# Optimization experiments

Hardware: AMD Instinct MI355X
Metric: run time of the kernel (lower is better)

Reference implementation:

```python
import jax, jax.numpy as jnp
import numpy as np

TEMPERATURE = 0.1
NUM_GROUPS = 1024  # must match fill_max of `groups`


def setup_inputs() -> dict:
    key = jax.random.key(0)
    k1, k2, k3 = jax.random.split(key, 3)
    B, N, D = 16, 16384, 128
    embeddings = jax.random.normal(k1, (B, N, D), dtype=jnp.float32)
    groups = jax.random.randint(k2, (B, N), 0, NUM_GROUPS, dtype=jnp.int32)
    mask = jax.random.randint(k3, (B, N), 0, 2, dtype=jnp.int32).astype(bool)
    return {"embeddings": embeddings, "groups": groups, "mask": mask}


def reference(embeddings, groups, mask):
    # Vectorized equivalent of the per-group python loop:
    # sort nodes by group, positives = roll-by-1 within each group block,
    # negatives = uniform sample from the complement of the anchor's group.
    B, N, D = embeddings.shape
    G = NUM_GROUPS
    emb = embeddings.reshape(B * N, D)
    g = groups.reshape(B * N)
    m = mask.reshape(B * N)
    total = B * N

    # masked-out nodes get sentinel group G -> sorted to the tail, excluded everywhere
    g_eff = jnp.where(m, g, G).astype(jnp.int32)
    order = jnp.argsort(g_eff)            # stable sort by group
    sg = g_eff[order]                     # sorted group labels
    counts = jax.ops.segment_sum(jnp.ones(total, jnp.int32), g_eff,
                                 num_segments=G + 1)
    starts = jnp.searchsorted(sg, jnp.arange(G + 1, dtype=jnp.int32))
    valid_total = total - counts[G]       # number of unmasked nodes

    gi = sg                               # group of element at each sorted position
    cnt = counts[gi]
    st = starts[gi]
    local = jnp.arange(total, dtype=jnp.int32) - st
    # positive partner: previous element in group, wrapping (torch.roll shifts=1)
    partner_local = jnp.mod(local - 1, jnp.maximum(cnt, 1))
    pos_idx = order[st + partner_local]
    anchor_idx = order

    # negative: uniform index into complement (all unmasked nodes not in group gi)
    comp = jnp.maximum(valid_total - cnt, 1)
    u = jax.random.uniform(jax.random.key(42), (total,))
    r = jnp.minimum((u * comp.astype(jnp.float32)).astype(jnp.int32), comp - 1)
    neg_pos = jnp.where(r < st, r, r + cnt)          # skip this group's block
    neg_idx = order[jnp.clip(neg_pos, 0, total - 1)]

    valid = (gi < G) & (cnt >= 2) & ((valid_total - cnt) > 0)

    a = emb[anchor_idx]
    p = emb[pos_idx]
    n = emb[neg_idx]
    pos_score = jnp.sum(a * p, axis=1) / TEMPERATURE
    neg_score = jnp.sum(a * n, axis=1) / TEMPERATURE
    # CE with label 0 over logits [pos, neg]: -log_softmax(...)[0]
    loss_i = jnp.logaddexp(pos_score, neg_score) - pos_score
    vw = valid.astype(loss_i.dtype)
    loss = jnp.sum(loss_i * vw) / jnp.maximum(jnp.sum(vw), 1.0)
    return loss
```

## Files before the change

kernel.cpp:

```cpp
#include <hip/hip_runtime.h>
#include <stdint.h>

#define TOTAL  262144
#define HALF   131072
#define G      1024
#define NBINS  1025
#define NCHUNK 512
#define CHUNK  512

#define OFF_COUNTS 0
#define OFF_STARTS 8192
#define OFF_FLAG   16384
#define OFF_VT     16388
#define OFF_LOSS   16392
#define OFF_VALID  16400
#define OFF_ORDER  16448
#define OFF_GHIST  1065024

__device__ __forceinline__ void threefry2x32(uint32_t k0, uint32_t k1,
                                             uint32_t& x0, uint32_t& x1) {
  uint32_t ks0 = k0, ks1 = k1, ks2 = k0 ^ k1 ^ 0x1BD11BDAu;
#define TF_RND(R) { x0 += x1; x1 = (x1 << (R)) | (x1 >> (32 - (R))); x1 ^= x0; }
  x0 += ks0; x1 += ks1;
  TF_RND(13) TF_RND(15) TF_RND(26) TF_RND(6)
  x0 += ks1; x1 += ks2 + 1u;
  TF_RND(17) TF_RND(29) TF_RND(16) TF_RND(24)
  x0 += ks2; x1 += ks0 + 2u;
  TF_RND(13) TF_RND(15) TF_RND(26) TF_RND(6)
  x0 += ks0; x1 += ks1 + 3u;
  TF_RND(17) TF_RND(29) TF_RND(16) TF_RND(24)
  x0 += ks1; x1 += ks2 + 4u;
  TF_RND(13) TF_RND(15) TF_RND(26) TF_RND(6)
  x0 += ks2; x1 += ks0 + 5u;
#undef TF_RND
}

__device__ __forceinline__ int load_mask(const void* mask, int is8, int j) {
  return is8 ? (int)((const unsigned char*)mask)[j] : ((const int*)mask)[j];
}

__global__ void k_probe_mask(const unsigned char* mb, int* flag) {
  int t = threadIdx.x;
  if ((t & 3) != 0 && mb[t] != 0) atomicOr(flag, 1);
}

__global__ __launch_bounds__(CHUNK) void k_hist(const int* __restrict__ groups,
                                                const void* __restrict__ mask,
                                                const int* __restrict__ flag,
                                                int* __restrict__ counts,
                                                int* __restrict__ ghist) {
  __shared__ int h[NBINS];
  int t = threadIdx.x;
  for (int b = t; b < NBINS; b += CHUNK) h[b] = 0;
  __syncthreads();
  int is8 = *flag;
  int j = blockIdx.x * CHUNK + t;
  int m = load_mask(mask, is8, j);
  int g = m ? groups[j] : G;
  atomicAdd(&h[g], 1);
  __syncthreads();
  for (int b = t; b < NBINS; b += CHUNK) {
    int v = h[b];
    ghist[b * NCHUNK + blockIdx.x] = v;
    if (v) atomicAdd(&counts[b], v);
  }
}

__global__ __launch_bounds__(64) void k_scan(const int* __restrict__ counts,
                                             int* __restrict__ starts,
                                             int* __restrict__ vt) {
  int l = threadIdx.x;
  int c[16];
  int s = 0;
#pragma unroll
  for (int k = 0; k < 16; k++) { c[k] = counts[l * 16 + k]; s += c[k]; }
  int incl = s;
  for (int d = 1; d < 64; d <<= 1) {
    int tt = __shfl_up(incl, d);
    if (l >= d) incl += tt;
  }
  int run = incl - s;
#pragma unroll
  for (int k = 0; k < 16; k++) { starts[l * 16 + k] = run; run += c[k]; }
  if (l == 63) starts[1024] = run;
  if (l == 0) *vt = TOTAL - counts[1024];
}

__global__ __launch_bounds__(256) void k_rebase(const int* __restrict__ starts,
                                                int* __restrict__ ghist) {
  int wave = threadIdx.x >> 6, lane = threadIdx.x & 63;
  int g = blockIdx.x * 4 + wave;
  if (g >= NBINS) return;
  int* row = ghist + g * NCHUNK;
  int v[8];
  int s = 0;
  int bi = lane * 8;
#pragma unroll
  for (int k = 0; k < 8; k++) { v[k] = row[bi + k]; s += v[k]; }
  int incl = s;
  for (int d = 1; d < 64; d <<= 1) {
    int tt = __shfl_up(incl, d);
    if (lane >= d) incl += tt;
  }
  int run = starts[g] + (incl - s);
#pragma unroll
  for (int k = 0; k < 8; k++) { int tt = v[k]; row[bi + k] = run; run += tt; }
}

__global__ __launch_bounds__(CHUNK) void k_scatter(const int* __restrict__ groups,
                                                   const void* __restrict__ mask,
                                                   const int* __restrict__ flag,
                                                   const int* __restrict__ ghist,
                                                   int* __restrict__ order) {
  __shared__ int gl[CHUNK];
  int t = threadIdx.x;
  int is8 = *flag;
  int j = blockIdx.x * CHUNK + t;
  int m = load_mask(mask, is8, j);
  int g = m ? groups[j] : G;
  gl[t] = g;
  __syncthreads();
  int rank = 0;
  for (int t2 = 0; t2 < t; t2++)
    rank += (gl[t2] == g) ? 1 : 0;
  int pos = ghist[g * NCHUNK + blockIdx.x] + rank;
  order[pos] = j;
}

__global__ __launch_bounds__(256) void k_main(const float* __restrict__ emb,
                                              const int* __restrict__ groups,
                                              const void* __restrict__ mask,
                                              const int* __restrict__ flag,
                                              const int* __restrict__ counts,
                                              const int* __restrict__ starts,
                                              const int* __restrict__ vtp,
                                              const int* __restrict__ order,
                                              double* __restrict__ lossAcc,
                                              double* __restrict__ validAcc) {
  __shared__ int mA[256], mP[256], mN[256], mV[256];
  int t = threadIdx.x;
  int i = blockIdx.x * 256 + t;
  int is8 = *flag;
  int j = order[i];
  int mm = load_mask(mask, is8, j);
  int g = mm ? groups[j] : G;
  int cnt = counts[g], st = starts[g];
  int local = i - st;
  int partner = (local == 0) ? (cnt - 1) : (local - 1);
  int pos_idx = order[st + partner];

  uint32_t x0, x1;
  if (i < HALF) { x0 = (uint32_t)i; x1 = (uint32_t)(i + HALF); }
  else          { x0 = (uint32_t)(i - HALF); x1 = (uint32_t)i; }
  threefry2x32(0u, 42u, x0, x1);
  uint32_t bits = (i < HALF) ? x0 : x1;
  float u = __uint_as_float((bits >> 9) | 0x3F800000u) - 1.0f;

  int vt = *vtp;
  int compi = vt - cnt;
  int comp = compi > 1 ? compi : 1;
  int r = (int)(u * (float)comp);
  int cm1 = comp - 1;
  if (r > cm1) r = cm1;
  int neg_pos = (r < st) ? r : (r + cnt);
  if (neg_pos < 0) neg_pos = 0;
  if (neg_pos > TOTAL - 1) neg_pos = TOTAL - 1;
  int neg_idx = order[neg_pos];
  int valid = (g < G) && (cnt >= 2) && (compi > 0);

  mA[t] = j; mP[t] = pos_idx; mN[t] = neg_idx; mV[t] = valid;
  __syncthreads();

  int wave = t >> 6, lane = t & 63;
  int sg = lane >> 3;
  int sl = lane & 7;
  const float4* e4 = (const float4*)emb;
  float lsum = 0.f, vsum = 0.f;
#pragma unroll 2
  for (int it = 0; it < 8; it++) {
    int mi = wave * 64 + it * 8 + sg;
    int ai = mA[mi], pi = mP[mi], ni = mN[mi], vv = mV[mi];
    const float4* ar = e4 + (size_t)ai * 32 + sl * 4;
    const float4* pr = e4 + (size_t)pi * 32 + sl * 4;
    const float4* nr = e4 + (size_t)ni * 32 + sl * 4;
    float ap = 0.f, an = 0.f;
#pragma unroll
    for (int k = 0; k < 4; k++) {
      float4 av = ar[k];
      float4 pv = pr[k];
      float4 nv = nr[k];
      ap += av.x * pv.x + av.y * pv.y + av.z * pv.z + av.w * pv.w;
      an += av.x * nv.x + av.y * nv.y + av.z * nv.z + av.w * nv.w;
    }
    ap += __shfl_xor(ap, 4); an += __shfl_xor(an, 4);
    ap += __shfl_xor(ap, 2); an += __shfl_xor(an, 2);
    ap += __shfl_xor(ap, 1); an += __shfl_xor(an, 1);
    if (vv && sl == 0) {
      float ps = ap * 10.0f, ns = an * 10.0f;
      float dd = ns - ps;
      float li = fmaxf(dd, 0.0f) + log1pf(expf(-fabsf(dd)));
      lsum += li; vsum += 1.0f;
    }
  }
  for (int d = 32; d >= 1; d >>= 1) {
    lsum += __shfl_xor(lsum, d);
    vsum += __shfl_xor(vsum, d);
  }
  if (lane == 0) {
    atomicAdd(lossAcc, (double)lsum);
    atomicAdd(validAcc, (double)vsum);
  }
}

__global__ void k_final(const double* lossAcc, const double* validAcc, float* out) {
  double v = *validAcc;
  if (v < 1.0) v = 1.0;
  out[0] = (float)(*lossAcc / v);
}

extern "C" void kernel_launch(void* const* d_in, const int* in_sizes, int n_in,
                              void* d_out, int out_size, void* d_ws, size_t ws_size,
                              hipStream_t stream) {
  const float* emb = (const float*)d_in[0];
  const int* groups = (const int*)d_in[1];
  const void* mask = d_in[2];
  float* out = (float*)d_out;

  char* ws = (char*)d_ws;
  int* counts = (int*)(ws + OFF_COUNTS);
  int* starts = (int*)(ws + OFF_STARTS);
  int* flag = (int*)(ws + OFF_FLAG);
  int* vt = (int*)(ws + OFF_VT);
  double* lossAcc = (double*)(ws + OFF_LOSS);
  double* validAcc = (double*)(ws + OFF_VALID);
  int* order = (int*)(ws + OFF_ORDER);
  int* ghist = (int*)(ws + OFF_GHIST);

  hipMemsetAsync(ws, 0, 16408, stream);

  k_probe_mask<<<1, 1024, 0, stream>>>((const unsigned char*)mask, flag);
  k_hist<<<NCHUNK, CHUNK, 0, stream>>>(groups, mask, flag, counts, ghist);
  k_scan<<<1, 64, 0, stream>>>(counts, starts, vt);
  k_rebase<<<(NBINS + 3) / 4, 256, 0, stream>>>(starts, ghist);
  k_scatter<<<NCHUNK, CHUNK, 0, stream>>>(groups, mask, flag, ghist, order);
  k_main<<<TOTAL / 256, 256, 0, stream>>>(emb, groups, mask, flag, counts, starts,
                                          vt, order, lossAcc, validAcc);
  k_final<<<1, 1, 0, stream>>>(lossAcc, validAcc, out);
}
```

Before: 322.0 us.

## Inline mask probe, ballot-based scatter ranks, shuffle-reuse positive rows in main

Removes the separate mask-probe kernel and detects the mask byte width per wave with a ballot inside each kernel. The O(n) per-thread shared-memory rank loop in scatter becomes a wave match built from 11 bit ballots plus per-wave shared histograms. The main kernel now handles 128 anchors per block. It reuses the previous anchor's row via shuffles as the positive when the partner is adjacent, which removes most positive-row gathers, and it reduces partial sums per block before one atomic. This trades more blocks and shuffle work for fewer launches, fewer global loads and less serial ranking work.

```diff
diff --git a/kernel.cpp b/kernel.cpp
--- a/kernel.cpp
+++ b/kernel.cpp
@@ -10,7 +10,6 @@
 
 #define OFF_COUNTS 0
 #define OFF_STARTS 8192
-#define OFF_FLAG   16384
 #define OFF_VT     16388
 #define OFF_LOSS   16392
 #define OFF_VALID  16400
@@ -39,21 +38,22 @@
   return is8 ? (int)((const unsigned char*)mask)[j] : ((const int*)mask)[j];
 }
 
-__global__ void k_probe_mask(const unsigned char* mb, int* flag) {
-  int t = threadIdx.x;
-  if ((t & 3) != 0 && mb[t] != 0) atomicOr(flag, 1);
+__device__ __forceinline__ int detect_is8(const void* mask) {
+  int lane = threadIdx.x & 63;
+  uchar4 p = ((const uchar4*)mask)[lane];
+  unsigned long long bal = __ballot((p.y | p.z | p.w) != 0);
+  return bal != 0ull;
 }
 
 __global__ __launch_bounds__(CHUNK) void k_hist(const int* __restrict__ groups,
                                                 const void* __restrict__ mask,
-                                                const int* __restrict__ flag,
                                                 int* __restrict__ counts,
                                                 int* __restrict__ ghist) {
   __shared__ int h[NBINS];
   int t = threadIdx.x;
+  int is8 = detect_is8(mask);
   for (int b = t; b < NBINS; b += CHUNK) h[b] = 0;
   __syncthreads();
-  int is8 = *flag;
   int j = blockIdx.x * CHUNK + t;
   int m = load_mask(mask, is8, j);
   int g = m ? groups[j] : G;
@@ -109,20 +109,29 @@
 
 __global__ __launch_bounds__(CHUNK) void k_scatter(const int* __restrict__ groups,
                                                    const void* __restrict__ mask,
-                                                   const int* __restrict__ flag,
                                                    const int* __restrict__ ghist,
                                                    int* __restrict__ order) {
-  __shared__ int gl[CHUNK];
+  __shared__ int h[8][NBINS];
   int t = threadIdx.x;
-  int is8 = *flag;
+  int wave = t >> 6, lane = t & 63;
+  int is8 = detect_is8(mask);
   int j = blockIdx.x * CHUNK + t;
   int m = load_mask(mask, is8, j);
   int g = m ? groups[j] : G;
-  gl[t] = g;
-  __syncthreads();
-  int rank = 0;
-  for (int t2 = 0; t2 < t; t2++)
-    rank += (gl[t2] == g) ? 1 : 0;
+  for (int idx = t; idx < 8 * NBINS; idx += CHUNK) ((int*)h)[idx] = 0;
+  __syncthreads();
+  unsigned long long mm = ~0ull;
+#pragma unroll
+  for (int b = 0; b < 11; b++) {
+    unsigned long long bal = __ballot(((g >> b) & 1) != 0);
+    mm &= ((g >> b) & 1) ? bal : ~bal;
+  }
+  unsigned long long lt = (1ull << lane) - 1ull;
+  int lanerank = __popcll(mm & lt);
+  if (lanerank == 0) h[wave][g] = __popcll(mm);
+  __syncthreads();
+  int rank = lanerank;
+  for (int w = 0; w < wave; w++) rank += h[w][g];
   int pos = ghist[g * NCHUNK + blockIdx.x] + rank;
   order[pos] = j;
 }
@@ -130,72 +139,93 @@
 __global__ __launch_bounds__(256) void k_main(const float* __restrict__ emb,
                                               const int* __restrict__ groups,
                                               const void* __restrict__ mask,
-                                              const int* __restrict__ flag,
                                               const int* __restrict__ counts,
                                               const int* __restrict__ starts,
                                               const int* __restrict__ vtp,
                                               const int* __restrict__ order,
                                               double* __restrict__ lossAcc,
                                               double* __restrict__ validAcc) {
-  __shared__ int mA[256], mP[256], mN[256], mV[256];
+  __shared__ int mA[128], mP[128], mN[128], mF[128];
+  __shared__ float bl[4], bv[4];
   int t = threadIdx.x;
-  int i = blockIdx.x * 256 + t;
-  int is8 = *flag;
-  int j = order[i];
-  int mm = load_mask(mask, is8, j);
-  int g = mm ? groups[j] : G;
-  int cnt = counts[g], st = starts[g];
-  int local = i - st;
-  int partner = (local == 0) ? (cnt - 1) : (local - 1);
-  int pos_idx = order[st + partner];
-
-  uint32_t x0, x1;
-  if (i < HALF) { x0 = (uint32_t)i; x1 = (uint32_t)(i + HALF); }
-  else          { x0 = (uint32_t)(i - HALF); x1 = (uint32_t)i; }
-  threefry2x32(0u, 42u, x0, x1);
-  uint32_t bits = (i < HALF) ? x0 : x1;
-  float u = __uint_as_float((bits >> 9) | 0x3F800000u) - 1.0f;
-
-  int vt = *vtp;
-  int compi = vt - cnt;
-  int comp = compi > 1 ? compi : 1;
-  int r = (int)(u * (float)comp);
-  int cm1 = comp - 1;
-  if (r > cm1) r = cm1;
-  int neg_pos = (r < st) ? r : (r + cnt);
-  if (neg_pos < 0) neg_pos = 0;
-  if (neg_pos > TOTAL - 1) neg_pos = TOTAL - 1;
-  int neg_idx = order[neg_pos];
-  int valid = (g < G) && (cnt >= 2) && (compi > 0);
-
-  mA[t] = j; mP[t] = pos_idx; mN[t] = neg_idx; mV[t] = valid;
-  __syncthreads();
-
   int wave = t >> 6, lane = t & 63;
-  int sg = lane >> 3;
-  int sl = lane & 7;
+  int is8 = detect_is8(mask);
+  int P0 = blockIdx.x * 128;
+
+  if (lane < 32) {
+    int i = P0 + wave * 32 + lane;
+    int j = order[i];
+    int mm2 = load_mask(mask, is8, j);
+    int g = mm2 ? groups[j] : G;
+    int cnt = counts[g], st = starts[g];
+    int local = i - st;
+    int partner_pos = (local == 0) ? (st + cnt - 1) : (i - 1);
+    int pos_idx = order[partner_pos];
+
+    uint32_t x0, x1;
+    if (i < HALF) { x0 = (uint32_t)i; x1 = (uint32_t)(i + HALF); }
+    else          { x0 = (uint32_t)(i - HALF); x1 = (uint32_t)i; }
+    threefry2x32(0u, 42u, x0, x1);
+    uint32_t bits = (i < HALF) ? x0 : x1;
+    float u = __uint_as_float((bits >> 9) | 0x3F800000u) - 1.0f;
+
+    int vt = *vtp;
+    int compi = vt - cnt;
+    int comp = compi > 1 ? compi : 1;
+    int r = (int)(u * (float)comp);
+    int cm1 = comp - 1;
+    if (r > cm1) r = cm1;
+    int neg_pos = (r < st) ? r : (r + cnt);
+    if (neg_pos < 0) neg_pos = 0;
+    if (neg_pos > TOTAL - 1) neg_pos = TOTAL - 1;
+    int neg_idx = order[neg_pos];
+    int valid = (g < G) && (cnt >= 2) && (compi > 0);
+    int shufok = (partner_pos == i - 1);
+
+    int slot = wave * 32 + lane;
+    mA[slot] = j; mP[slot] = pos_idx; mN[slot] = neg_idx;
+    mF[slot] = valid | (shufok << 1);
+  }
+  __syncthreads();
+
+  int sg = lane >> 3, sl = lane & 7;
   const float4* e4 = (const float4*)emb;
   float lsum = 0.f, vsum = 0.f;
-#pragma unroll 2
-  for (int it = 0; it < 8; it++) {
-    int mi = wave * 64 + it * 8 + sg;
-    int ai = mA[mi], pi = mP[mi], ni = mN[mi], vv = mV[mi];
+#pragma unroll 1
+  for (int it = 0; it < 4; it++) {
+    int slot = wave * 32 + it * 8 + sg;
+    int ai = mA[slot], pi = mP[slot], ni = mN[slot], fl = mF[slot];
     const float4* ar = e4 + (size_t)ai * 32 + sl * 4;
-    const float4* pr = e4 + (size_t)pi * 32 + sl * 4;
     const float4* nr = e4 + (size_t)ni * 32 + sl * 4;
-    float ap = 0.f, an = 0.f;
-#pragma unroll
-    for (int k = 0; k < 4; k++) {
-      float4 av = ar[k];
-      float4 pv = pr[k];
-      float4 nv = nr[k];
-      ap += av.x * pv.x + av.y * pv.y + av.z * pv.z + av.w * pv.w;
-      an += av.x * nv.x + av.y * nv.y + av.z * nv.z + av.w * nv.w;
+    float4 a0 = ar[0], a1 = ar[1], a2 = ar[2], a3 = ar[3];
+    float4 n0 = nr[0], n1 = nr[1], n2 = nr[2], n3 = nr[3];
+    float4 p0, p1, p2, p3;
+    p0.x = __shfl_up(a0.x, 8); p0.y = __shfl_up(a0.y, 8);
+    p0.z = __shfl_up(a0.z, 8); p0.w = __shfl_up(a0.w, 8);
+    p1.x = __shfl_up(a1.x, 8); p1.y = __shfl_up(a1.y, 8);
+    p1.z = __shfl_up(a1.z, 8); p1.w = __shfl_up(a1.w, 8);
+    p2.x = __shfl_up(a2.x, 8); p2.y = __shfl_up(a2.y, 8);
+    p2.z = __shfl_up(a2.z, 8); p2.w = __shfl_up(a2.w, 8);
+    p3.x = __shfl_up(a3.x, 8); p3.y = __shfl_up(a3.y, 8);
+    p3.z = __shfl_up(a3.z, 8); p3.w = __shfl_up(a3.w, 8);
+    int useshuf = (sg > 0) && (fl & 2);
+    if (!useshuf) {
+      const float4* pr = e4 + (size_t)pi * 32 + sl * 4;
+      p0 = pr[0]; p1 = pr[1]; p2 = pr[2]; p3 = pr[3];
     }
+    float ap0 = a0.x*p0.x + a0.y*p0.y + a0.z*p0.z + a0.w*p0.w
+              + a1.x*p1.x + a1.y*p1.y + a1.z*p1.z + a1.w*p1.w;
+    float ap1 = a2.x*p2.x + a2.y*p2.y + a2.z*p2.z + a2.w*p2.w
+              + a3.x*p3.x + a3.y*p3.y + a3.z*p3.z + a3.w*p3.w;
+    float an0 = a0.x*n0.x + a0.y*n0.y + a0.z*n0.z + a0.w*n0.w
+              + a1.x*n1.x + a1.y*n1.y + a1.z*n1.z + a1.w*n1.w;
+    float an1 = a2.x*n2.x + a2.y*n2.y + a2.z*n2.z + a2.w*n2.w
+              + a3.x*n3.x + a3.y*n3.y + a3.z*n3.z + a3.w*n3.w;
+    float ap = ap0 + ap1, an = an0 + an1;
     ap += __shfl_xor(ap, 4); an += __shfl_xor(an, 4);
     ap += __shfl_xor(ap, 2); an += __shfl_xor(an, 2);
     ap += __shfl_xor(ap, 1); an += __shfl_xor(an, 1);
-    if (vv && sl == 0) {
+    if ((fl & 1) && sl == 0) {
       float ps = ap * 10.0f, ns = an * 10.0f;
       float dd = ns - ps;
       float li = fmaxf(dd, 0.0f) + log1pf(expf(-fabsf(dd)));
@@ -206,9 +236,13 @@
     lsum += __shfl_xor(lsum, d);
     vsum += __shfl_xor(vsum, d);
   }
-  if (lane == 0) {
-    atomicAdd(lossAcc, (double)lsum);
-    atomicAdd(validAcc, (double)vsum);
+  if (lane == 0) { bl[wave] = lsum; bv[wave] = vsum; }
+  __syncthreads();
+  if (t == 0) {
+    float L = bl[0] + bl[1] + bl[2] + bl[3];
+    float V = bv[0] + bv[1] + bv[2] + bv[3];
+    atomicAdd(lossAcc, (double)L);
+    atomicAdd(validAcc, (double)V);
   }
 }
 
@@ -229,7 +263,6 @@
   char* ws = (char*)d_ws;
   int* counts = (int*)(ws + OFF_COUNTS);
   int* starts = (int*)(ws + OFF_STARTS);
-  int* flag = (int*)(ws + OFF_FLAG);
   int* vt = (int*)(ws + OFF_VT);
   double* lossAcc = (double*)(ws + OFF_LOSS);
   double* validAcc = (double*)(ws + OFF_VALID);
@@ -238,12 +271,11 @@
 
   hipMemsetAsync(ws, 0, 16408, stream);
 
-  k_probe_mask<<<1, 1024, 0, stream>>>((const unsigned char*)mask, flag);
-  k_hist<<<NCHUNK, CHUNK, 0, stream>>>(groups, mask, flag, counts, ghist);
+  k_hist<<<NCHUNK, CHUNK, 0, stream>>>(groups, mask, counts, ghist);
   k_scan<<<1, 64, 0, stream>>>(counts, starts, vt);
   k_rebase<<<(NBINS + 3) / 4, 256, 0, stream>>>(starts, ghist);
-  k_scatter<<<NCHUNK, CHUNK, 0, stream>>>(groups, mask, flag, ghist, order);
-  k_main<<<TOTAL / 256, 256, 0, stream>>>(emb, groups, mask, flag, counts, starts,
+  k_scatter<<<NCHUNK, CHUNK, 0, stream>>>(groups, mask, ghist, order);
+  k_main<<<TOTAL / 128, 256, 0, stream>>>(emb, groups, mask, counts, starts,
                                           vt, order, lossAcc, validAcc);
   k_final<<<1, 1, 0, stream>>>(lossAcc, validAcc, out);
 }
```

New measurement: 318.1 us. No clear change (-1.2%).
